# Performance work log

Measured on AMD Instinct MI355X. Metric: run time of the kernel, lower is better.

The kernel has to match this reference:

```python
import jax, jax.numpy as jnp
import numpy as np

N, T, D, H, E, ED = 4096, 16, 5, 128, 32768, 32

def _leaky(x):
    return jnp.where(x >= 0, x, 0.2 * x)

def _lstm(x, Wih, Whh, bih, bhh):
    # x: [N, T, D] -> hidden sequence [N, T, H]; PyTorch gate order i,f,g,o
    pre = jnp.einsum('ntd,gd->tng', x, Wih) + bih + bhh  # [T, N, 4H]
    Hd = Whh.shape[1]
    def step(carry, p):
        h, c = carry
        g = p + h @ Whh.T
        i, f, gg, o = jnp.split(g, 4, axis=-1)
        c = jax.nn.sigmoid(f) * c + jax.nn.sigmoid(i) * jnp.tanh(gg)
        h = jax.nn.sigmoid(o) * jnp.tanh(c)
        return (h, c), h
    z = jnp.zeros((x.shape[0], Hd), x.dtype)
    _, hs = jax.lax.scan(step, (z, z), pre)
    return jnp.swapaxes(hs, 0, 1)

def _sire(x, src, dst, efeat, Wq, bq, Wk, bk, We, be, Wr, br):
    # SIREConv with agg_type='sum': m = LeakyReLU(eq[dst]+ek[src]+e); sum over in-edges; then linear_relation
    eq = x @ Wq.T + bq            # [N, T, H]
    ek = x @ Wk.T + bk            # [N, T, H]
    e = efeat @ We.T + be         # [E, H]
    m = _leaky(eq[dst] + ek[src] + e[:, None, :])  # [E, T, H]
    ft = jax.ops.segment_sum(m, dst, num_segments=x.shape[0])  # [N, T, H]
    return ft @ Wr.T + br

def _forward(stock_features, srcs, dsts, efeats, sire_ps, lstm_p, attn_p, mlp_p):
    sf = stock_features / jnp.mean(stock_features, axis=1, keepdims=True)
    sr = _lstm(sf, *lstm_p)  # [N, T, H]
    outs = [sr]
    for s, d, ef, p in zip(srcs, dsts, efeats, sire_ps):
        outs.append(_sire(sr, s, d, ef, *p))
    cat = jnp.concatenate(outs, axis=-1)  # [N, T, 4H]
    aw = jax.nn.softmax(cat @ attn_p[0].T + attn_p[1], axis=-2)  # softmax over time
    pooled = jnp.sum(cat * aw, axis=-2)   # [N, 4H]
    W1, b1, W2, b2 = mlp_p
    h = _leaky(pooled @ W1.T + b1)
    out = _leaky(h @ W2.T + b2)           # [N, 1]
    return out / sf[:, -1, 0:1] - 1.0


def setup_inputs() -> dict:
    key = jax.random.key(0)
    ks = iter(jax.random.split(key, 64))
    def nrm(shape, s=0.05):
        return jax.random.normal(next(ks), shape, jnp.float32) * s
    inp = {}
    inp['stock_features'] = jax.random.uniform(next(ks), (N, T, D), jnp.float32) + 0.5
    for g in ['wiki', 'industry', 'corr']:
        inp[g + '_src'] = jax.random.randint(next(ks), (E,), 0, N, jnp.int32)
        inp[g + '_dst'] = jax.random.randint(next(ks), (E,), 0, N, jnp.int32)
        inp[g + '_efeat'] = nrm((E, ED), 1.0)
        inp[g + '_Wq'] = nrm((H, H)); inp[g + '_bq'] = nrm((H,))
        inp[g + '_Wk'] = nrm((H, H)); inp[g + '_bk'] = nrm((H,))
        inp[g + '_We'] = nrm((H, ED)); inp[g + '_be'] = nrm((H,))
        inp[g + '_Wr'] = nrm((H, H)); inp[g + '_br'] = nrm((H,))
    inp['lstm_Wih'] = nrm((4 * H, D)); inp['lstm_Whh'] = nrm((4 * H, H))
    inp['lstm_bih'] = nrm((4 * H,)); inp['lstm_bhh'] = nrm((4 * H,))
    inp['attn_W'] = nrm((1, 4 * H)); inp['attn_b'] = nrm((1,))
    inp['mlp_W1'] = nrm((H, 4 * H)); inp['mlp_b1'] = nrm((H,))
    inp['mlp_W2'] = nrm((1, H)); inp['mlp_b2'] = nrm((1,))
    return inp


def reference(stock_features, wiki_src, wiki_dst, wiki_efeat,
              wiki_Wq, wiki_bq, wiki_Wk, wiki_bk, wiki_We, wiki_be, wiki_Wr, wiki_br,
              industry_src, industry_dst, industry_efeat,
              industry_Wq, industry_bq, industry_Wk, industry_bk, industry_We, industry_be, industry_Wr, industry_br,
              corr_src, corr_dst, corr_efeat,
              corr_Wq, corr_bq, corr_Wk, corr_bk, corr_We, corr_be, corr_Wr, corr_br,
              lstm_Wih, lstm_Whh, lstm_bih, lstm_bhh,
              attn_W, attn_b, mlp_W1, mlp_b1, mlp_W2, mlp_b2):
    srcs = (wiki_src, industry_src, corr_src)
    dsts = (wiki_dst, industry_dst, corr_dst)
    efeats = (wiki_efeat, industry_efeat, corr_efeat)
    sire_ps = ((wiki_Wq, wiki_bq, wiki_Wk, wiki_bk, wiki_We, wiki_be, wiki_Wr, wiki_br),
               (industry_Wq, industry_bq, industry_Wk, industry_bk, industry_We, industry_be, industry_Wr, industry_br),
               (corr_Wq, corr_bq, corr_Wk, corr_bk, corr_We, corr_be, corr_Wr, corr_br))
    return _forward(stock_features, srcs, dsts, efeats, sire_ps,
                    (lstm_Wih, lstm_Whh, lstm_bih, lstm_bhh),
                    (attn_W, attn_b), (mlp_W1, mlp_b1, mlp_W2, mlp_b2))
```

## Files before the change

### kernel.cpp

```cpp
#include <hip/hip_runtime.h>
#include <cstdint>
#include <cstddef>

#define NS 4096
#define TS 16
#define DF 5
#define HD 128
#define EE 32768
#define EDD 32

typedef _Float16 h16;
typedef __attribute__((ext_vector_type(8))) _Float16 f16x8;
typedef __attribute__((ext_vector_type(2))) __fp16 fp16x2_n;
typedef __attribute__((ext_vector_type(4))) float f32x4;

__device__ __forceinline__ float sigmoidf_(float x){ return 1.f/(1.f+__expf(-x)); }
__device__ __forceinline__ float tanhf_(float x){ return 1.f - 2.f/(1.f+__expf(2.f*x)); }
__device__ __forceinline__ float leaky_(float x){ return x >= 0.f ? x : 0.2f*x; }

__device__ __forceinline__ unsigned pkh(float a, float b){
  union { fp16x2_n h; unsigned u; } x;
  x.h = __builtin_amdgcn_cvt_pkrtz(a, b);
  return x.u;
}
__device__ __forceinline__ void unpkh(unsigned u, float& a, float& b){
  union { unsigned u; fp16x2_n h; } x; x.u = u;
  a = (float)x.h.x; b = (float)x.h.y;
}
__device__ __forceinline__ f16x8 ld_h8(const h16* p){
  union { uint4 u; f16x8 v; } x; x.u = *(const uint4*)p; return x.v;
}

template<int AH, int CH>
__device__ __forceinline__ void gemm_dev(const void* Av, int lda,
    const float* __restrict__ Bp, int ldb, const float* __restrict__ bp,
    void* Cv, int ldc, int K, int act, size_t m0,
    h16* Asb, h16* Bsb)
{
  int tid = threadIdx.x;
  int wv = tid>>6, lane = tid&63, lm = lane&15, lq = lane>>4;
  f32x4 acc[2][8];
  #pragma unroll
  for (int mt=0;mt<2;mt++)
    #pragma unroll
    for (int nt=0;nt<8;nt++)
      acc[mt][nt] = (f32x4){0.f,0.f,0.f,0.f};

  for (int k0=0; k0<K; k0+=32){
    if (AH){
      const h16* A = (const h16*)Av;
      #pragma unroll
      for (int rep=0;rep<2;rep++){
        int idx = tid + rep*256;
        int row = idx>>2, c8 = idx&3;
        *(uint4*)&Asb[row*40 + c8*8] = *(const uint4*)&A[(m0+row)*(size_t)lda + k0 + c8*8];
      }
    } else {
      const float* A = (const float*)Av;
      #pragma unroll
      for (int rep=0;rep<4;rep++){
        int idx = tid + rep*256;
        int row = idx>>3, c4 = idx&7;
        float4 a = *(const float4*)&A[(m0+row)*(size_t)lda + k0 + c4*4];
        *(uint2*)&Asb[row*40 + c4*4] = make_uint2(pkh(a.x,a.y), pkh(a.z,a.w));
      }
    }
    #pragma unroll
    for (int rep=0;rep<4;rep++){
      int idx = tid + rep*256;
      int row = idx>>3, c4 = idx&7;
      float4 b = *(const float4*)&Bp[(size_t)row*ldb + k0 + c4*4];
      *(uint2*)&Bsb[row*40 + c4*4] = make_uint2(pkh(b.x,b.y), pkh(b.z,b.w));
    }
    __syncthreads();
    f16x8 afr[2], bfr[8];
    #pragma unroll
    for (int mt=0;mt<2;mt++)
      afr[mt] = ld_h8(&Asb[(wv*32 + mt*16 + lm)*40 + lq*8]);
    #pragma unroll
    for (int nt=0;nt<8;nt++)
      bfr[nt] = ld_h8(&Bsb[(nt*16 + lm)*40 + lq*8]);
    #pragma unroll
    for (int mt=0;mt<2;mt++)
      #pragma unroll
      for (int nt=0;nt<8;nt++)
        acc[mt][nt] = __builtin_amdgcn_mfma_f32_16x16x32_f16(afr[mt], bfr[nt], acc[mt][nt], 0,0,0);
    __syncthreads();
  }

  #pragma unroll
  for (int mt=0;mt<2;mt++){
    #pragma unroll
    for (int nt=0;nt<8;nt++){
      int col = nt*16 + lm;
      float bv = bp[col];
      #pragma unroll
      for (int i=0;i<4;i++){
        float o = acc[mt][nt][i] + bv;
        if (act) o = leaky_(o);
        size_t ridx = (m0 + wv*32 + mt*16 + lq*4 + i)*(size_t)ldc + col;
        if (CH) ((h16*)Cv)[ridx] = (h16)o;
        else    ((float*)Cv)[ridx] = o;
      }
    }
  }
}

__device__ void lstm8_dev(int blk, const float* __restrict__ sf,
                          const h16* __restrict__ WhhH,
                          const float* __restrict__ Wih, const float* __restrict__ bih,
                          const float* __restrict__ bhh, h16* __restrict__ cat,
                          char* smem)
{
  float* gates = (float*)smem;
  h16* hbuf = (h16*)(smem+16512);
  float* sfb = (float*)(smem+16512+2176);
  int tid = threadIdx.x;
  int n0 = blk*8;
  int wv = tid>>6, lane = tid&63, lm = lane&15, lq = lane>>4;

  f16x8 bfr[8][4];
  #pragma unroll
  for (int nt=0;nt<8;nt++){
    int g = wv*128 + nt*16 + lm;
    #pragma unroll
    for (int kt=0;kt<4;kt++)
      bfr[nt][kt] = *(const f16x8*)&WhhH[g*128 + kt*32 + lq*8];
  }

  int j = tid & 127;
  int rb = tid >> 7;
  float wih[4][5]; float bsum[4];
  #pragma unroll
  for (int gi=0; gi<4; gi++){
    int gc = gi*128 + j;
    #pragma unroll
    for (int d=0; d<5; d++) wih[gi][d] = Wih[gc*5+d];
    bsum[gi] = bih[gc] + bhh[gc];
  }
  float cst[4] = {0.f,0.f,0.f,0.f};

  for (int i=tid;i<544;i+=256) ((unsigned*)hbuf)[i] = 0;
  for (int i=tid;i<640;i+=256) sfb[i] = sf[(size_t)n0*80 + i];
  __syncthreads();

  f16x8 zf = {0,0,0,0,0,0,0,0};
  for (int t=0;t<16;t++){
    f16x8 af[4];
    #pragma unroll
    for (int kt=0;kt<4;kt++)
      af[kt] = (lm < 8) ? *(const f16x8*)&hbuf[lm*136 + kt*32 + lq*8] : zf;
    #pragma unroll
    for (int nt=0;nt<8;nt++){
      f32x4 acc = {0.f,0.f,0.f,0.f};
      #pragma unroll
      for (int kt=0;kt<4;kt++)
        acc = __builtin_amdgcn_mfma_f32_16x16x32_f16(af[kt], bfr[nt][kt], acc, 0,0,0);
      if (lq < 2){
        int col = wv*128 + nt*16 + lm;
        #pragma unroll
        for (int i=0;i<4;i++)
          gates[(lq*4+i)*516 + col] = acc[i];
      }
    }
    __syncthreads();
    #pragma unroll
    for (int q=0;q<4;q++){
      int r = rb + 2*q;
      const float* s = &sfb[r*80 + t*5];
      float pre[4];
      #pragma unroll
      for (int gi=0;gi<4;gi++){
        float a = bsum[gi];
        #pragma unroll
        for (int d=0;d<5;d++) a = fmaf(s[d], wih[gi][d], a);
        pre[gi] = a + gates[r*516 + gi*128 + j];
      }
      float iv = sigmoidf_(pre[0]);
      float fv = sigmoidf_(pre[1]);
      float gv = tanhf_(pre[2]);
      float ov = sigmoidf_(pre[3]);
      float c = fv*cst[q] + iv*gv;
      cst[q] = c;
      float h = ov*tanhf_(c);
      h16 hh = (h16)h;
      hbuf[r*136 + j] = hh;
      cat[(size_t)((n0+r)*16 + t)*512 + j] = hh;
    }
    __syncthreads();
  }
}

__global__ __launch_bounds__(256)
void k_prolog(const float* __restrict__ x, float* __restrict__ sf,
              const float* __restrict__ Whh, h16* __restrict__ whhH,
              int* __restrict__ cnt)
{
  int b = blockIdx.x, tid = threadIdx.x;
  if (b < 80){
    int id = b*256 + tid;
    if (id < NS*DF){
      int n = id / DF, d = id % DF;
      const float* xp = x + (size_t)n*TS*DF + d;
      float s = 0.f;
      #pragma unroll
      for (int t=0;t<TS;t++) s += xp[t*DF];
      float inv = (float)TS / s;
      float* sp = sf + (size_t)n*TS*DF + d;
      #pragma unroll
      for (int t=0;t<TS;t++) sp[t*DF] = xp[t*DF]*inv;
    }
  } else if (b < 336){
    int i = (b-80)*256 + tid;
    whhH[i] = (h16)Whh[i];
  } else {
    int i = (b-336)*256 + tid;
    cnt[i] = 0;
  }
}

struct M1 {
  const float *sf, *Wih, *bih, *bhh;
  const h16* WhhH;
  h16* cat;
  const float *ef[3]; const float *We[3]; const float *be[3];
  h16* eeb;
  const int* dst[3];
  int* cnt;
};
__global__ __launch_bounds__(256,2)
void k_mega1(M1 p)
{
  __shared__ __align__(16) char smem[21504];
  int b = blockIdx.x;
  if (b < 512){
    lstm8_dev(b, p.sf, p.WhhH, p.Wih, p.bih, p.bhh, p.cat, smem);
  } else if (b < 1280){
    int idx = b - 512;
    int proj = idx % 3, mt = idx / 3;
    h16* Asb = (h16*)smem;
    h16* Bsb = Asb + 128*40;
    gemm_dev<0,1>(p.ef[proj], 32, p.We[proj], 32, p.be[proj],
                  p.eeb + (size_t)proj*EE*128, 128, 32, 0, (size_t)mt*128, Asb, Bsb);
  } else {
    int idx = b - 1280;
    int g = idx >> 7, blk = idx & 127;
    int e = blk*256 + threadIdx.x;
    atomicAdd(&p.cnt[g*4096 + p.dst[g][e]], 1);
  }
}

__global__ __launch_bounds__(1024)
void k_scan(const int* __restrict__ cnt_, int* __restrict__ rs_, int* __restrict__ woff_){
  __shared__ int buf[1024];
  int g = blockIdx.x;
  const int* cnt = cnt_ + g*4096;
  int* rs = rs_ + g*4097;
  int* woff = woff_ + g*4096;
  int tid = threadIdx.x;
  int b = tid*4;
  int v0=cnt[b],v1=cnt[b+1],v2=cnt[b+2],v3=cnt[b+3];
  int s = v0+v1+v2+v3;
  buf[tid]=s;
  __syncthreads();
  for (int off=1; off<1024; off<<=1){
    int t = (tid>=off) ? buf[tid-off] : 0;
    __syncthreads();
    buf[tid] += t;
    __syncthreads();
  }
  int excl = buf[tid] - s;
  rs[b+0]=excl; woff[b+0]=excl; excl+=v0;
  rs[b+1]=excl; woff[b+1]=excl; excl+=v1;
  rs[b+2]=excl; woff[b+2]=excl; excl+=v2;
  rs[b+3]=excl; woff[b+3]=excl;
  if (tid==1023) rs[4096]=excl+v3;
}

struct M2 {
  const h16* cat;
  const float* W[6]; const float* bias[6];
  h16* eqk;
  const int* dst[3];
  int* woff; int* eidx;
};
__global__ __launch_bounds__(256)
void k_mega2(M2 p)
{
  __shared__ __align__(16) h16 Asb[128*40];
  __shared__ __align__(16) h16 Bsb[128*40];
  int b = blockIdx.x;
  if (b < 3072){
    int proj = b % 6, mt = b / 6;
    gemm_dev<1,1>(p.cat, 512, p.W[proj], 128, p.bias[proj],
                  p.eqk + (size_t)proj*NS*TS*128, 128, 128, 0, (size_t)mt*128, Asb, Bsb);
  } else {
    int idx = b - 3072;
    int g = idx >> 7, blk = idx & 127;
    int e = blk*256 + threadIdx.x;
    int pos = atomicAdd(&p.woff[g*4096 + p.dst[g][e]], 1);
    p.eidx[g*EE + pos] = e;
  }
}

struct P3 { const int* p[3]; };
__global__ __launch_bounds__(256)
void k_edge(const h16* __restrict__ eqk, const h16* __restrict__ eeb,
            P3 src, const int* __restrict__ rs_, const int* __restrict__ eidx_,
            h16* __restrict__ ft_)
{
  int n = blockIdx.x;
  int g = blockIdx.y;
  const h16* eqb = eqk + (size_t)(2*g)  *NS*TS*128;
  const h16* ekb = eqk + (size_t)(2*g+1)*NS*TS*128;
  const h16* eeg = eeb + (size_t)g*EE*128;
  h16* ft = ft_ + (size_t)g*NS*TS*128;
  const int* srcp = src.p[g];
  const int* rs = rs_ + g*4097;
  const int* eidx = eidx_ + g*EE;
  int tid = threadIdx.x;
  int t = tid>>4, hb = (tid&15)*8;
  size_t own = ((size_t)(n*16+t))*128 + hb;
  f16x8 eqv = ld_h8(&eqb[own]);
  const f16x8 c02 = {(h16)0.2f,(h16)0.2f,(h16)0.2f,(h16)0.2f,
                     (h16)0.2f,(h16)0.2f,(h16)0.2f,(h16)0.2f};
  float acc[8];
  #pragma unroll
  for (int j=0;j<8;j++) acc[j]=0.f;
  int i0 = rs[n], i1 = rs[n+1];
  for (int i=i0;i<i1;i++){
    int e = eidx[i];
    int s = srcp[e];
    f16x8 kv = ld_h8(&ekb[((size_t)(s*16+t))*128 + hb]);
    f16x8 ev = ld_h8(&eeg[(size_t)e*128 + hb]);
    f16x8 x = eqv + kv + ev;
    f16x8 lk = __builtin_elementwise_max(x, x*c02);
    #pragma unroll
    for (int j=0;j<8;j++) acc[j] += (float)lk[j];
  }
  uint4 o;
  o.x = pkh(acc[0],acc[1]); o.y = pkh(acc[2],acc[3]);
  o.z = pkh(acc[4],acc[5]); o.w = pkh(acc[6],acc[7]);
  *(uint4*)&ft[own] = o;
}

struct WrP {
  const h16* A[3];
  const float* B[3]; const float* bias[3];
  h16* C[3];
};
__global__ __launch_bounds__(256)
void k_wr(WrP p)
{
  __shared__ __align__(16) h16 Asb[128*40];
  __shared__ __align__(16) h16 Bsb[128*40];
  int proj = blockIdx.x;
  size_t m0 = (size_t)blockIdx.y * 128;
  gemm_dev<1,1>(p.A[proj], 128, p.B[proj], 128, p.bias[proj],
                p.C[proj], 512, 128, 0, m0, Asb, Bsb);
}

__global__ __launch_bounds__(256)
void k_attn(const h16* __restrict__ cat, const float* __restrict__ attnW,
            const float* __restrict__ attnB, h16* __restrict__ pooled)
{
  __shared__ h16 ct[16*512];
  __shared__ float sred[4][16];
  int n = blockIdx.x, tid = threadIdx.x;
  {
    const uint4* srcp = (const uint4*)(cat + (size_t)n*8192);
    uint4* dstp = (uint4*)ct;
    for (int i=tid;i<1024;i+=256) dstp[i] = srcp[i];
  }
  __syncthreads();
  int c0 = tid*2;
  float w0 = attnW[c0], w1 = attnW[c0+1];
  const unsigned* ctu = (const unsigned*)ct;
  float loc[16];
  #pragma unroll
  for (int t=0;t<16;t++){
    float a,b; unpkh(ctu[t*256 + tid], a, b);
    loc[t] = a*w0 + b*w1;
  }
  #pragma unroll
  for (int t=0;t<16;t++){
    float v = loc[t];
    for (int off=1; off<64; off<<=1) v += __shfl_xor(v, off, 64);
    loc[t]=v;
  }
  int wave = tid >> 6, lane = tid & 63;
  if (lane==0){
    #pragma unroll
    for (int t=0;t<16;t++) sred[wave][t]=loc[t];
  }
  __syncthreads();
  float s[16]; float m=-1e30f;
  float ab = attnB[0];
  #pragma unroll
  for (int t=0;t<16;t++){ s[t] = sred[0][t]+sred[1][t]+sred[2][t]+sred[3][t] + ab; m = fmaxf(m, s[t]); }
  float sum=0.f;
  #pragma unroll
  for (int t=0;t<16;t++){ s[t] = __expf(s[t]-m); sum += s[t]; }
  float inv = 1.f/sum;
  float p0=0.f,p1=0.f;
  #pragma unroll
  for (int t=0;t<16;t++){
    float a = s[t]*inv;
    float x,y; unpkh(ctu[t*256 + tid], x, y);
    p0 = fmaf(x, a, p0); p1 = fmaf(y, a, p1);
  }
  ((unsigned*)pooled)[(size_t)n*256 + tid] = pkh(p0,p1);
}

__global__ __launch_bounds__(256)
void k_mlp(const h16* __restrict__ pooled, const float* __restrict__ W1,
           const float* __restrict__ b1, float* __restrict__ hmlp)
{
  __shared__ __align__(16) h16 Asb[128*40];
  __shared__ __align__(16) h16 Bsb[128*40];
  gemm_dev<1,0>(pooled, 512, W1, 512, b1, hmlp, 128, 512, 1,
                (size_t)blockIdx.x*128, Asb, Bsb);
}

__global__ __launch_bounds__(256)
void k_final(const float* __restrict__ hmlp, const float* __restrict__ W2,
             const float* __restrict__ b2, const float* __restrict__ sf,
             float* __restrict__ out)
{
  int tid = threadIdx.x;
  int n = blockIdx.x*4 + (tid>>6);
  int lane = tid & 63;
  const float* hp = hmlp + (size_t)n*128;
  float v = hp[lane]*W2[lane] + hp[64+lane]*W2[64+lane];
  for (int off=1; off<64; off<<=1) v += __shfl_xor(v, off, 64);
  if (lane==0){
    float o = v + b2[0];
    o = leaky_(o);
    out[n] = o / sf[(size_t)n*80 + 75] - 1.f;
  }
}

extern "C" void kernel_launch(void* const* d_in, const int* in_sizes, int n_in,
                              void* d_out, int out_size, void* d_ws, size_t ws_size,
                              hipStream_t stream)
{
  const float* x    = (const float*)d_in[0];
  const float* Wih  = (const float*)d_in[34];
  const float* Whh  = (const float*)d_in[35];
  const float* bih  = (const float*)d_in[36];
  const float* bhh  = (const float*)d_in[37];
  const float* attnW= (const float*)d_in[38];
  const float* attnB= (const float*)d_in[39];
  const float* W1   = (const float*)d_in[40];
  const float* b1   = (const float*)d_in[41];
  const float* W2   = (const float*)d_in[42];
  const float* b2   = (const float*)d_in[43];

  char* w = (char*)d_ws;
  size_t o = 0;
  h16* cat    = (h16*)(w+o); o += (size_t)NS*TS*512*2;
  h16* eqk    = (h16*)(w+o); o += (size_t)6*NS*TS*128*2;
  h16* eeb    = (h16*)(w+o); o += (size_t)3*EE*128*2;
  h16* ft     = (h16*)(w+o); o += (size_t)3*NS*TS*128*2;
  h16* pooled = (h16*)(w+o); o += (size_t)NS*512*2;
  float* sf   = (float*)(w+o); o += (size_t)NS*TS*DF*4;
  float* hmlp = (float*)(w+o); o += (size_t)NS*HD*4;
  h16* whhH = (h16*)(w+o); o += (size_t)512*128*2;
  int* cnt  = (int*)(w+o); o += 3*4096*4;
  int* rs   = (int*)(w+o); o += 3*4097*4;
  int* woff = (int*)(w+o); o += 3*4096*4;
  int* eidx = (int*)(w+o); o += (size_t)3*EE*4;

  P3 srcs = {{ (const int*)d_in[1], (const int*)d_in[12], (const int*)d_in[23] }};

  k_prolog<<<384, 256, 0, stream>>>(x, sf, Whh, whhH, cnt);

  {
    M1 p;
    p.sf = sf; p.Wih = Wih; p.bih = bih; p.bhh = bhh;
    p.WhhH = whhH; p.cat = cat; p.eeb = eeb; p.cnt = cnt;
    for (int g=0; g<3; g++){
      int base = 1 + g*11;
      p.ef[g] = (const float*)d_in[base+2];
      p.We[g] = (const float*)d_in[base+7];
      p.be[g] = (const float*)d_in[base+8];
      p.dst[g] = (const int*)d_in[base+1];
    }
    k_mega1<<<1664, 256, 0, stream>>>(p);
  }

  k_scan<<<3, 1024, 0, stream>>>(cnt, rs, woff);

  {
    M2 p;
    p.cat = cat; p.eqk = eqk; p.woff = woff; p.eidx = eidx;
    for (int g=0; g<3; g++){
      int base = 1 + g*11;
      p.W[2*g]      = (const float*)d_in[base+3];
      p.bias[2*g]   = (const float*)d_in[base+4];
      p.W[2*g+1]    = (const float*)d_in[base+5];
      p.bias[2*g+1] = (const float*)d_in[base+6];
      p.dst[g] = (const int*)d_in[base+1];
    }
    k_mega2<<<3456, 256, 0, stream>>>(p);
  }

  k_edge<<<dim3(NS,3), 256, 0, stream>>>(eqk, eeb, srcs, rs, eidx, ft);

  {
    WrP p;
    for (int g=0; g<3; g++){
      int base = 1 + g*11;
      p.A[g]    = ft + (size_t)g*NS*TS*128;
      p.B[g]    = (const float*)d_in[base+9];
      p.bias[g] = (const float*)d_in[base+10];
      p.C[g]    = cat + (size_t)(1+g)*128;
    }
    k_wr<<<dim3(3,512), 256, 0, stream>>>(p);
  }

  k_attn<<<NS, 256, 0, stream>>>(cat, attnW, attnB, pooled);
  k_mlp<<<32, 256, 0, stream>>>(pooled, W1, b1, hmlp);
  k_final<<<NS/4, 256, 0, stream>>>(hmlp, W2, b2, sf, (float*)d_out);
}
```

Measured before the change: 380.4 us.

## Stage GEMM fp16 epilogue through LDS and prefetch edge indices into shared memory

The fp16 GEMM epilogue now writes each tile into LDS first and then stores it to global memory as coalesced 16-byte rows, replacing scattered 2-byte stores. The edge-aggregation kernel loads the first 64 edge ids and their source ids into shared memory once per block, which takes the dependent eidx to srcp load chain out of the per-edge loop. The prolog kernel also reorders its block ranges so the counter zeroing runs first, and that zeroing now covers only 3*4096 entries behind a guard. The trade-off is extra LDS traffic and barriers in the epilogue plus one more barrier in the edge kernel.

Result: slower. 389.4 us (+2.4%).

```diff
diff --git a/kernel.cpp b/kernel.cpp
--- a/kernel.cpp
+++ b/kernel.cpp
@@ -88,19 +88,47 @@
     __syncthreads();
   }
 
-  #pragma unroll
-  for (int mt=0;mt<2;mt++){
-    #pragma unroll
-    for (int nt=0;nt<8;nt++){
-      int col = nt*16 + lm;
-      float bv = bp[col];
-      #pragma unroll
-      for (int i=0;i<4;i++){
-        float o = acc[mt][nt][i] + bv;
-        if (act) o = leaky_(o);
-        size_t ridx = (m0 + wv*32 + mt*16 + lq*4 + i)*(size_t)ldc + col;
-        if (CH) ((h16*)Cv)[ridx] = (h16)o;
-        else    ((float*)Cv)[ridx] = o;
+  if (CH){
+    h16* lds = Asb;
+    h16* C = (h16*)Cv;
+    #pragma unroll
+    for (int mt=0;mt<2;mt++){
+      __syncthreads();
+      h16* lws = lds + wv*2176;
+      #pragma unroll
+      for (int nt=0;nt<8;nt++){
+        int col = nt*16 + lm;
+        float bv = bp[col];
+        #pragma unroll
+        for (int i=0;i<4;i++){
+          float o = acc[mt][nt][i] + bv;
+          if (act) o = leaky_(o);
+          lws[(lq*4+i)*136 + col] = (h16)o;
+        }
+      }
+      __syncthreads();
+      #pragma unroll
+      for (int it=0; it<4; it++){
+        int q = tid + it*256;
+        int rr = q>>4, cc = q&15;
+        int wvv = rr>>4, r = rr&15;
+        uint4 v = *(const uint4*)&lds[wvv*2176 + r*136 + cc*8];
+        *(uint4*)&C[(m0 + wvv*32 + mt*16 + r)*(size_t)ldc + cc*8] = v;
+      }
+    }
+  } else {
+    #pragma unroll
+    for (int mt=0;mt<2;mt++){
+      #pragma unroll
+      for (int nt=0;nt<8;nt++){
+        int col = nt*16 + lm;
+        float bv = bp[col];
+        #pragma unroll
+        for (int i=0;i<4;i++){
+          float o = acc[mt][nt][i] + bv;
+          if (act) o = leaky_(o);
+          ((float*)Cv)[(m0 + wv*32 + mt*16 + lq*4 + i)*(size_t)ldc + col] = o;
+        }
       }
     }
   }
@@ -197,8 +225,11 @@
               int* __restrict__ cnt)
 {
   int b = blockIdx.x, tid = threadIdx.x;
-  if (b < 80){
-    int id = b*256 + tid;
+  if (b < 48){
+    int i = b*256 + tid;
+    if (i < 3*4096) cnt[i] = 0;
+  } else if (b < 128){
+    int id = (b-48)*256 + tid;
     if (id < NS*DF){
       int n = id / DF, d = id % DF;
       const float* xp = x + (size_t)n*TS*DF + d;
@@ -210,12 +241,9 @@
       #pragma unroll
       for (int t=0;t<TS;t++) sp[t*DF] = xp[t*DF]*inv;
     }
-  } else if (b < 336){
-    int i = (b-80)*256 + tid;
+  } else {
+    int i = (b-128)*256 + tid;
     whhH[i] = (h16)Whh[i];
-  } else {
-    int i = (b-336)*256 + tid;
-    cnt[i] = 0;
   }
 }
 
@@ -309,6 +337,7 @@
             P3 src, const int* __restrict__ rs_, const int* __restrict__ eidx_,
             h16* __restrict__ ft_)
 {
+  __shared__ int sl_e[64], sl_s[64];
   int n = blockIdx.x;
   int g = blockIdx.y;
   const h16* eqb = eqk + (size_t)(2*g)  *NS*TS*128;
@@ -319,6 +348,13 @@
   const int* rs = rs_ + g*4097;
   const int* eidx = eidx_ + g*EE;
   int tid = threadIdx.x;
+  int i0 = rs[n], i1 = rs[n+1];
+  int ne = i1 - i0;
+  if (tid < 64 && tid < ne){
+    int e = eidx[i0 + tid];
+    sl_e[tid] = e;
+    sl_s[tid] = srcp[e];
+  }
   int t = tid>>4, hb = (tid&15)*8;
   size_t own = ((size_t)(n*16+t))*128 + hb;
   f16x8 eqv = ld_h8(&eqb[own]);
@@ -327,10 +363,11 @@
   float acc[8];
   #pragma unroll
   for (int j=0;j<8;j++) acc[j]=0.f;
-  int i0 = rs[n], i1 = rs[n+1];
-  for (int i=i0;i<i1;i++){
-    int e = eidx[i];
-    int s = srcp[e];
+  __syncthreads();
+  for (int i=0;i<ne;i++){
+    int e, s;
+    if (i < 64){ e = sl_e[i]; s = sl_s[i]; }
+    else       { e = eidx[i0+i]; s = srcp[e]; }
     f16x8 kv = ld_h8(&ekb[((size_t)(s*16+t))*128 + hb]);
     f16x8 ev = ld_h8(&eeg[(size_t)e*128 + hb]);
     f16x8 x = eqv + kv + ev;
```
